# Performance work log

Hardware: AMD Instinct MI355X
Metric: run time of the kernel (lower is better)

The kernel has to match this reference:

```python
import jax, jax.numpy as jnp
import numpy as np

# ---- config (matches init_kwargs) ----
B, S, V = 8, 900, 11
H, NH, HD = 512, 8, 64          # hidden, heads, head_dim = H // NH
L = 2                            # num_layers
EXPANSION = 4.0
INNER = 1536                     # find_multiple(round(4.0 * 512 * 2/3), 256)
STEPS = 2                        # mcmc_num_steps
EPS = 1e-5                       # rms_norm_eps
THETA = 10000.0                  # rope_theta
ESCALE = float(np.sqrt(H))       # embed_scale = sqrt(hidden_size)
SCALE = 1.0 / float(np.sqrt(HD))


def rms_norm(x):
    return x * jax.lax.rsqrt(jnp.mean(x * x, axis=-1, keepdims=True) + EPS)


def rope_tables():
    inv_freq = 1.0 / (THETA ** (jnp.arange(0, HD, 2, dtype=jnp.float32) / HD))
    t = jnp.arange(S, dtype=jnp.float32)
    freqs = jnp.outer(t, inv_freq)                # (S, HD/2)
    emb = jnp.concatenate([freqs, freqs], axis=-1)  # (S, HD)
    return jnp.cos(emb), jnp.sin(emb)


def rotate_half(x):
    x1, x2 = jnp.split(x, 2, axis=-1)
    return jnp.concatenate([-x2, x1], axis=-1)


def apply_rope(q, k, cos, sin):
    cos = cos[None, :, None, :]  # (1,S,1,HD) broadcast over batch & heads
    sin = sin[None, :, None, :]
    return q * cos + rotate_half(q) * sin, k * cos + rotate_half(k) * sin


def block(h, qkv_w, o_w, gu_w, d_w, cos, sin):
    b, s, _ = h.shape
    qkv = (h @ qkv_w).reshape(b, s, 3 * NH, HD)
    q, k, v = qkv[:, :, :NH], qkv[:, :, NH:2 * NH], qkv[:, :, 2 * NH:]
    q, k = apply_rope(q, k, cos, sin)
    scores = jnp.einsum('bqhd,bkhd->bhqk', q, k) * SCALE
    attn = jax.nn.softmax(scores, axis=-1)
    out = jnp.einsum('bhqk,bkhd->bqhd', attn, v).reshape(b, s, NH * HD)
    h = rms_norm(h + out @ o_w)                   # post-norm residual
    gu = h @ gu_w
    gate, up = gu[..., :INNER], gu[..., INNER:]
    h = rms_norm(h + (jax.nn.silu(gate) * up) @ d_w)
    return h


def energy(logits, embed_w, energy_w, qkv_w, o_w, gu_w, d_w, input_emb, cos, sin):
    probs = jax.nn.softmax(logits, axis=-1)       # soft token distribution
    h = input_emb + ESCALE * (probs @ embed_w)    # soft embedding
    for i in range(L):
        h = block(h, qkv_w[i], o_w[i], gu_w[i], d_w[i], cos, sin)
    return jnp.sum(h @ energy_w)                  # scalar energy


def setup_inputs() -> dict:
    key = jax.random.key(0)
    ks = jax.random.split(key, 8)
    inputs = jax.random.randint(ks[0], (B, S), 0, V, dtype=jnp.int64)
    puzzle_identifiers = jax.random.randint(ks[1], (B,), 0, 1, dtype=jnp.int64)
    init_std = 1.0 / ESCALE
    embed_w = jax.random.normal(ks[2], (V, H), jnp.float32) * init_std
    energy_w = jax.random.normal(ks[3], (H, 1), jnp.float32) * 0.02
    qkv_w = jax.random.normal(ks[4], (L, H, 3 * NH * HD), jnp.float32) * 0.02
    o_w = jax.random.normal(ks[5], (L, NH * HD, H), jnp.float32) * 0.02
    gu_w = jax.random.normal(ks[6], (L, H, 2 * INNER), jnp.float32) * 0.02
    d_w = jax.random.normal(ks[7], (L, INNER, H), jnp.float32) * 0.02
    alpha = jnp.asarray(100.0, jnp.float32)       # mcmc_step_size
    return {"inputs": inputs, "puzzle_identifiers": puzzle_identifiers,
            "embed_w": embed_w, "energy_w": energy_w, "qkv_w": qkv_w,
            "o_w": o_w, "gu_w": gu_w, "d_w": d_w, "alpha": alpha}


def reference(inputs, puzzle_identifiers, embed_w, energy_w, qkv_w, o_w, gu_w, d_w, alpha):
    cos, sin = rope_tables()
    input_emb = ESCALE * embed_w[inputs]          # (B,S,H)
    a = jnp.maximum(alpha, 1e-4)                  # torch.clamp(alpha, min=1e-4)
    logits = jnp.zeros((inputs.shape[0], S, V), jnp.float32)
    egrad = jax.grad(energy)
    for _ in range(STEPS):                        # MCMC energy-descent loop
        g = egrad(logits, embed_w, energy_w, qkv_w, o_w, gu_w, d_w, input_emb, cos, sin)
        logits = logits - a * g
    return logits
```

## Files before the change

### kernel.cpp

```cpp
#include <hip/hip_runtime.h>
#include <math.h>

#define B_ 8
#define S_ 900
#define V_ 11
#define H_ 512
#define NH_ 8
#define HD_ 64
#define INNER_ 1536
#define STEPS_ 2
#define NTOK (B_*S_)
#define EPS_ 1e-5f
#define THETA_ 10000.0f
#define ESCALE_ 22.627416997969522f
#define SCALE_ 0.125f
#define PT_ 68

typedef __attribute__((ext_vector_type(8))) short bh8;
typedef __attribute__((ext_vector_type(4))) float f32x4;
typedef __attribute__((ext_vector_type(4))) unsigned short us4;

union bfu { bh8 v; unsigned short s[8]; us4 q[2]; };

__device__ inline unsigned short f2bf(float x) {
  unsigned u = __builtin_bit_cast(unsigned, x);
  return (unsigned short)((u + 0x7FFFu + ((u >> 16) & 1u)) >> 16);
}
__device__ inline float b2f(unsigned short s) {
  return __builtin_bit_cast(float, (unsigned)s << 16);
}

__device__ inline void gld16(const unsigned short* g, unsigned short* l) {
  __builtin_amdgcn_global_load_lds(
      (const __attribute__((address_space(1))) void*)(g),
      (__attribute__((address_space(3))) void*)(l), 16, 0, 0);
}

__device__ inline bh8 lds16(const unsigned short* p) {
  bfu u;
  u.q[0] = *(const us4*)p;
  u.q[1] = *(const us4*)(p + 4);
  return u.v;
}
__device__ inline void sts16(unsigned short* p, bfu u) {
  *(us4*)p = u.q[0];
  *(us4*)(p + 4) = u.q[1];
}

__device__ inline float wave_sum64(float x) {
#pragma unroll
  for (int off = 32; off > 0; off >>= 1) x += __shfl_xor(x, off, 64);
  return x;
}

__device__ inline float quad_sum(float x) {
  x += __shfl_xor(x, 1, 64);
  x += __shfl_xor(x, 2, 64);
  return x;
}


__global__ void k_zero(float* p, int n) {
  int i = blockIdx.x * blockDim.x + threadIdx.x;
  if (i < n) p[i] = 0.f;
}

__global__ void k_rope_tables(float* cs, float* sn) {
  int idx = blockIdx.x * blockDim.x + threadIdx.x;
  if (idx >= S_ * 32) return;
  int s = idx >> 5, i = idx & 31;
  float freq = powf(THETA_, -(float)i / 32.0f);
  float ang = (float)s * freq;
  cs[idx] = cosf(ang);
  sn[idx] = sinf(ang);
}

__global__ void k_softmax_logits(const float* __restrict__ logits, float* __restrict__ P) {
  int t = blockIdx.x * blockDim.x + threadIdx.x;
  if (t >= NTOK) return;
  float x[V_];
  float m = -1e30f;
#pragma unroll
  for (int v = 0; v < V_; ++v) { x[v] = logits[t * V_ + v]; m = fmaxf(m, x[v]); }
  float ssum = 0.f;
#pragma unroll
  for (int v = 0; v < V_; ++v) { x[v] = expf(x[v] - m); ssum += x[v]; }
  float inv = 1.f / ssum;
#pragma unroll
  for (int v = 0; v < V_; ++v) P[t * V_ + v] = x[v] * inv;
}

__global__ void k_h0(const float* __restrict__ P, const float* __restrict__ E,
                     const int* __restrict__ inp, float* __restrict__ h0,
                     unsigned short* __restrict__ h016) {
  int t = blockIdx.x;
  int tid = threadIdx.x;
  __shared__ float p[V_];
  __shared__ int iw;
  if (tid < V_) p[tid] = P[t * V_ + tid];
  if (tid == 0) iw = inp[t];
  __syncthreads();
  for (int h = tid; h < H_; h += blockDim.x) {
    float acc = E[iw * H_ + h];
#pragma unroll
    for (int v = 0; v < V_; ++v) acc += p[v] * E[v * H_ + h];
    float val = ESCALE_ * acc;
    h0[(size_t)t * H_ + h] = val;
    h016[(size_t)t * H_ + h] = f2bf(val);
  }
}

__global__ void k_gfill(const float* __restrict__ ew, float* __restrict__ G) {
  int idx = blockIdx.x * blockDim.x + threadIdx.x;
  if (idx < NTOK * H_) G[idx] = ew[idx & (H_ - 1)];
}

__global__ void k_cast8(const float* __restrict__ X, unsigned short* __restrict__ Y, int n8) {
  int i = blockIdx.x * blockDim.x + threadIdx.x;
  if (i >= n8) return;
  const float4* p = (const float4*)(X + (size_t)i * 8);
  float4 a = p[0], b = p[1];
  bfu o;
  o.s[0] = f2bf(a.x); o.s[1] = f2bf(a.y); o.s[2] = f2bf(a.z); o.s[3] = f2bf(a.w);
  o.s[4] = f2bf(b.x); o.s[5] = f2bf(b.y); o.s[6] = f2bf(b.z); o.s[7] = f2bf(b.w);
  *(bh8*)(Y + (size_t)i * 8) = o.v;
}


__global__ void k_wt(const float* __restrict__ W, unsigned short* __restrict__ WT, int K, int N) {
  __shared__ float t[32][33];
  int k0 = blockIdx.y * 32, n0 = blockIdx.x * 32;
  int tx = threadIdx.x, ty = threadIdx.y;
#pragma unroll
  for (int i = 0; i < 4; ++i)
    t[ty + 8 * i][tx] = W[(size_t)(k0 + ty + 8 * i) * N + n0 + tx];
  __syncthreads();
#pragma unroll
  for (int i = 0; i < 4; ++i)
    WT[(size_t)(n0 + ty + 8 * i) * K + k0 + tx] = f2bf(t[tx][ty + 8 * i]);
}


template <int SILU_A, int ADD, int CBF>
__global__ __launch_bounds__(256) void k_gemm(const unsigned short* __restrict__ A16,
                                              const unsigned short* __restrict__ Bt,
                                              const float* __restrict__ Dm,
                                              float* __restrict__ Cf,
                                              unsigned short* __restrict__ C16,
                                              int M, int N, int K, int lda) {
  __shared__ unsigned short As[64][32];
  __shared__ unsigned short Bs[128][32];
  int tid = threadIdx.x;
  int m0 = blockIdx.y * 64, n0 = blockIdx.x * 128;
  int wid = tid >> 6, lane = tid & 63;
  int wr = (wid >> 1) * 32, wc = (wid & 1) * 64;
  int lr = lane & 15, lg = lane >> 4;
  int srow = lane >> 2, sck = (lane & 3) * 8;
  f32x4 acc[2][4] = {};
  for (int k0 = 0; k0 < K; k0 += 32) {
    __syncthreads();
    if (SILU_A) {
      int row = tid >> 2, ck = (tid & 3) * 8;
      int gr = m0 + row; gr = gr < M ? gr : M - 1;
      const unsigned short* src = &A16[(size_t)gr * lda + k0 + ck];
      bfu pa;
#pragma unroll
      for (int j = 0; j < 8; ++j) {
        float g = b2f(src[j]), u = b2f(src[INNER_ + j]);
        pa.s[j] = f2bf((g / (1.f + __expf(-g))) * u);
      }
      *(bh8*)&As[row][ck] = pa.v;
    } else {
      int row = wid * 16 + srow;
      int gr = m0 + row; gr = gr < M ? gr : M - 1;
      gld16(&A16[(size_t)gr * lda + k0 + sck], &As[wid * 16][0]);
    }
#pragma unroll
    for (int i = 0; i < 2; ++i) {
      int bb = wid * 2 + i;
      gld16(&Bt[(size_t)(n0 + bb * 16 + srow) * K + k0 + sck], &Bs[bb * 16][0]);
    }
    __syncthreads();
    bh8 av[2], bv[4];
#pragma unroll
    for (int fr = 0; fr < 2; ++fr) av[fr] = *(const bh8*)&As[wr + fr * 16 + lr][lg * 8];
#pragma unroll
    for (int fc = 0; fc < 4; ++fc) bv[fc] = *(const bh8*)&Bs[wc + fc * 16 + lr][lg * 8];
#pragma unroll
    for (int fr = 0; fr < 2; ++fr)
#pragma unroll
      for (int fc = 0; fc < 4; ++fc)
        acc[fr][fc] = __builtin_amdgcn_mfma_f32_16x16x32_bf16(av[fr], bv[fc], acc[fr][fc], 0, 0, 0);
  }
#pragma unroll
  for (int fr = 0; fr < 2; ++fr) {
    int r0 = m0 + wr + fr * 16 + lg * 4;
#pragma unroll
    for (int i = 0; i < 4; ++i) {
      int gr = r0 + i;
      if (gr >= M) continue;
#pragma unroll
      for (int fc = 0; fc < 4; ++fc) {
        int gc = n0 + wc + fc * 16 + lr;
        float out = acc[fr][fc][i];
        if (ADD) out += Dm[(size_t)gr * N + gc];
        if (CBF) C16[(size_t)gr * N + gc] = f2bf(out);
        else Cf[(size_t)gr * N + gc] = out;
      }
    }
  }
}


template <int BWD>
__global__ void k_rope(unsigned short* __restrict__ Q, const float* __restrict__ cs,
                       const float* __restrict__ sn) {
  int idx = blockIdx.x * blockDim.x + threadIdx.x;
  if (idx >= NTOK * NH_ * 2 * 32) return;
  int i = idx & 31;
  int h = (idx >> 5) & (NH_ - 1);
  int part = (idx >> 8) & 1;
  int t = idx >> 9;
  int s = t % S_;
  float c = cs[s * 32 + i], sv = sn[s * 32 + i];
  size_t base = ((size_t)t * 3 * NH_ + part * NH_ + h) * HD_;
  float x1 = b2f(Q[base + i]), x2 = b2f(Q[base + 32 + i]);
  if (!BWD) {
    Q[base + i] = f2bf(x1 * c - x2 * sv);
    Q[base + 32 + i] = f2bf(x2 * c + x1 * sv);
  } else {
    Q[base + i] = f2bf(x1 * c + x2 * sv);
    Q[base + 32 + i] = f2bf(x2 * c - x1 * sv);
  }
}


__global__ __launch_bounds__(256) void k_attn_fwd3(const unsigned short* __restrict__ QKV,
                                                   unsigned short* __restrict__ AO,
                                                   float* __restrict__ MB,
                                                   float* __restrict__ LB) {
  __shared__ unsigned short Ks[64][PT_];
  __shared__ unsigned short VT[64][PT_];
  __shared__ unsigned short Ps[4][16][PT_];
  int tid = threadIdx.x;
  int h = blockIdx.y, b = blockIdx.z;
  int w = tid >> 6, lane = tid & 63;
  int lr = lane & 15, lg = lane >> 4;
  int q0 = blockIdx.x * 64 + w * 16;

  bh8 qf[2];
  {
    int qr = q0 + lr; if (qr >= S_) qr = S_ - 1;
    const unsigned short* qp = &QKV[((size_t)(b * S_ + qr) * 24 + h) * 64 + lg * 8];
    qf[0] = *(const bh8*)qp;
    qf[1] = *(const bh8*)(qp + 32);
  }
  f32x4 accO[4] = {};
  float m[4], lsum[4];
#pragma unroll
  for (int i = 0; i < 4; ++i) { m[i] = -1e30f; lsum[i] = 0.f; }

  for (int kt = 0; kt < S_; kt += 64) {
    __syncthreads();
    {
      int r = tid >> 2, c0 = (tid & 3) * 16;
      int src = kt + r;
      size_t ts = (size_t)b * S_ + (src < S_ ? src : S_ - 1);
      const unsigned short* gp = &QKV[(ts * 24 + 8 + h) * 64 + c0];
      bfu p0, p1;
      p0.v = *(const bh8*)gp;
      p1.v = *(const bh8*)(gp + 8);
      sts16(&Ks[r][c0], p0);
      sts16(&Ks[r][c0 + 8], p1);
    }
    {
      int d0 = (tid & 15) * 4, k0r = (tid >> 4) * 4;
      us4 rv[4];
#pragma unroll
      for (int j = 0; j < 4; ++j) {
        int src = kt + k0r + j;
        size_t ts = (size_t)b * S_ + (src < S_ ? src : S_ - 1);
        rv[j] = *(const us4*)&QKV[(ts * 24 + 16 + h) * 64 + d0];
      }
#pragma unroll
      for (int dd = 0; dd < 4; ++dd) {
        us4 pk = {rv[0][dd], rv[1][dd], rv[2][dd], rv[3][dd]};
        *(us4*)&VT[d0 + dd][k0r] = pk;
      }
    }
    __syncthreads();
    f32x4 accS[4] = {};
#pragma unroll
    for (int ks = 0; ks < 2; ++ks)
#pragma unroll
      for (int fk = 0; fk < 4; ++fk)
        accS[fk] = __builtin_amdgcn_mfma_f32_16x16x32_bf16(qf[ks], lds16(&Ks[fk * 16 + lr][ks * 32 + lg * 8]), accS[fk], 0, 0, 0);
    float sc[4][4], pmax[4];
#pragma unroll
    for (int i = 0; i < 4; ++i) pmax[i] = -1e30f;
#pragma unroll
    for (int fk = 0; fk < 4; ++fk)
#pragma unroll
      for (int i = 0; i < 4; ++i) {
        float s = accS[fk][i] * SCALE_;
        if (kt + fk * 16 + lr >= S_) s = -1e30f;
        sc[fk][i] = s;
        pmax[i] = fmaxf(pmax[i], s);
      }
#pragma unroll
    for (int i = 0; i < 4; ++i) {
      float v = pmax[i];
      v = fmaxf(v, __shfl_xor(v, 1, 64));
      v = fmaxf(v, __shfl_xor(v, 2, 64));
      v = fmaxf(v, __shfl_xor(v, 4, 64));
      v = fmaxf(v, __shfl_xor(v, 8, 64));
      pmax[i] = v;
    }
    float psum[4];
#pragma unroll
    for (int i = 0; i < 4; ++i) {
      float mn = fmaxf(m[i], pmax[i]);
      float eo = __expf(m[i] - mn);
      m[i] = mn;
      lsum[i] *= eo;
#pragma unroll
      for (int fd = 0; fd < 4; ++fd) accO[fd][i] *= eo;
      psum[i] = 0.f;
    }
#pragma unroll
    for (int fk = 0; fk < 4; ++fk)
#pragma unroll
      for (int i = 0; i < 4; ++i) {
        float p = __expf(sc[fk][i] - m[i]);
        sc[fk][i] = p;
        psum[i] += p;
      }
#pragma unroll
    for (int i = 0; i < 4; ++i) {
      float v = psum[i];
      v += __shfl_xor(v, 1, 64);
      v += __shfl_xor(v, 2, 64);
      v += __shfl_xor(v, 4, 64);
      v += __shfl_xor(v, 8, 64);
      lsum[i] += v;
    }
#pragma unroll
    for (int fk = 0; fk < 4; ++fk)
#pragma unroll
      for (int i = 0; i < 4; ++i)
        Ps[w][lg * 4 + i][fk * 16 + lr] = f2bf(sc[fk][i]);
#pragma unroll
    for (int ks = 0; ks < 2; ++ks) {
      bh8 ap = lds16(&Ps[w][lr][ks * 32 + lg * 8]);
#pragma unroll
      for (int fd = 0; fd < 4; ++fd)
        accO[fd] = __builtin_amdgcn_mfma_f32_16x16x32_bf16(ap, lds16(&VT[fd * 16 + lr][ks * 32 + lg * 8]), accO[fd], 0, 0, 0);
    }
  }
#pragma unroll
  for (int i = 0; i < 4; ++i) {
    int q = q0 + lg * 4 + i;
    if (q < S_) {
      float linv = 1.f / lsum[i];
      size_t obase = (size_t)(b * S_ + q) * H_ + h * 64;
#pragma unroll
      for (int fd = 0; fd < 4; ++fd) AO[obase + fd * 16 + lr] = f2bf(accO[fd][i] * linv);
      if (lr == 0) {
        MB[((size_t)b * NH_ + h) * S_ + q] = m[i];
        LB[((size_t)b * NH_ + h) * S_ + q] = linv;
      }
    }
  }
}

__global__ __launch_bounds__(256) void k_delta(const unsigned short* __restrict__ O,
                                               const unsigned short* __restrict__ dO,
                                               float* __restrict__ DB) {
  int tid = threadIdx.x;
  int h = blockIdx.y, b = blockIdx.z;
  int r = blockIdx.x * 64 + (tid >> 2), part = tid & 3;
  if (r >= S_) return;
  size_t base = (size_t)(b * S_ + r) * H_ + h * 64 + part * 16;
  bfu o0, o1, d0, d1;
  o0.v = *(const bh8*)&O[base];  o1.v = *(const bh8*)&O[base + 8];
  d0.v = *(const bh8*)&dO[base]; d1.v = *(const bh8*)&dO[base + 8];
  float s = 0.f;
#pragma unroll
  for (int j = 0; j < 8; ++j)
    s += b2f(o0.s[j]) * b2f(d0.s[j]) + b2f(o1.s[j]) * b2f(d1.s[j]);
  s = quad_sum(s);
  if (part == 0) DB[((size_t)b * NH_ + h) * S_ + r] = s;
}

__global__ __launch_bounds__(256) void k_attn_bwd_dq3(const unsigned short* __restrict__ QKV,
                                                      const unsigned short* __restrict__ dO,
                                                      const float* __restrict__ MB,
                                                      const float* __restrict__ LB,
                                                      const float* __restrict__ DB,
                                                      unsigned short* __restrict__ dQKV) {
  __shared__ unsigned short Ks[64][PT_];
  __shared__ unsigned short Vs[64][PT_];
  __shared__ unsigned short KT[64][PT_];
  __shared__ unsigned short Ps[4][16][PT_];
  int tid = threadIdx.x;
  int h = blockIdx.y, b = blockIdx.z;
  int w = tid >> 6, lane = tid & 63;
  int lr = lane & 15, lg = lane >> 4;
  int q0 = blockIdx.x * 64 + w * 16;
  size_t sbase = ((size_t)b * NH_ + h) * S_;

  bh8 qf[2], dof[2];
  {
    int qr = q0 + lr; if (qr >= S_) qr = S_ - 1;
    const unsigned short* qp = &QKV[((size_t)(b * S_ + qr) * 24 + h) * 64 + lg * 8];
    const unsigned short* dp = &dO[(size_t)(b * S_ + qr) * H_ + h * 64 + lg * 8];
    qf[0] = *(const bh8*)qp;  qf[1] = *(const bh8*)(qp + 32);
    dof[0] = *(const bh8*)dp; dof[1] = *(const bh8*)(dp + 32);
  }
  float mrow[4], lrow[4], drow[4];
#pragma unroll
  for (int i = 0; i < 4; ++i) {
    int q = q0 + lg * 4 + i; if (q >= S_) q = S_ - 1;
    mrow[i] = MB[sbase + q];
    lrow[i] = LB[sbase + q];
    drow[i] = DB[sbase + q];
  }
  f32x4 accQ[4] = {};

  for (int kt = 0; kt < S_; kt += 64) {
    __syncthreads();
    {
      int r = tid >> 2, c0 = (tid & 3) * 16;
      int src = kt + r;
      bool vld = src < S_;
      size_t ts = (size_t)b * S_ + (vld ? src : S_ - 1);
      const unsigned short* kp = &QKV[(ts * 24 + 8 + h) * 64 + c0];
      bfu p0{}, p1{}, p2{}, p3{};
      if (vld) {
        p0.v = *(const bh8*)kp;
        p1.v = *(const bh8*)(kp + 8);
        p2.v = *(const bh8*)(kp + 512);
        p3.v = *(const bh8*)(kp + 520);
      }
      sts16(&Ks[r][c0], p0); sts16(&Ks[r][c0 + 8], p1);
      sts16(&Vs[r][c0], p2); sts16(&Vs[r][c0 + 8], p3);
    }
    {
      int d0 = (tid & 15) * 4, k0r = (tid >> 4) * 4;
      us4 rv[4];
#pragma unroll
      for (int j = 0; j < 4; ++j) {
        int src = kt + k0r + j;
        bool vld = src < S_;
        size_t ts = (size_t)b * S_ + (vld ? src : S_ - 1);
        us4 t = *(const us4*)&QKV[(ts * 24 + 8 + h) * 64 + d0];
        if (!vld) t = us4{0, 0, 0, 0};
        rv[j] = t;
      }
#pragma unroll
      for (int dd = 0; dd < 4; ++dd) {
        us4 pk = {rv[0][dd], rv[1][dd], rv[2][dd], rv[3][dd]};
        *(us4*)&KT[d0 + dd][k0r] = pk;
      }
    }
    __syncthreads();
    f32x4 aS[4] = {}, aD[4] = {};
#pragma unroll
    for (int ks = 0; ks < 2; ++ks)
#pragma unroll
      for (int fk = 0; fk < 4; ++fk) {
        aS[fk] = __builtin_amdgcn_mfma_f32_16x16x32_bf16(qf[ks], lds16(&Ks[fk * 16 + lr][ks * 32 + lg * 8]), aS[fk], 0, 0, 0);
        aD[fk] = __builtin_amdgcn_mfma_f32_16x16x32_bf16(dof[ks], lds16(&Vs[fk * 16 + lr][ks * 32 + lg * 8]), aD[fk], 0, 0, 0);
      }
#pragma unroll
    for (int fk = 0; fk < 4; ++fk)
#pragma unroll
      for (int i = 0; i < 4; ++i) {
        float p = __expf(aS[fk][i] * SCALE_ - mrow[i]) * lrow[i];
        float ds = p * (aD[fk][i] - drow[i]);
        Ps[w][lg * 4 + i][fk * 16 + lr] = f2bf(ds);
      }
#pragma unroll
    for (int ks = 0; ks < 2; ++ks) {
      bh8 ap = lds16(&Ps[w][lr][ks * 32 + lg * 8]);
#pragma unroll
      for (int fd = 0; fd < 4; ++fd)
        accQ[fd] = __builtin_amdgcn_mfma_f32_16x16x32_bf16(ap, lds16(&KT[fd * 16 + lr][ks * 32 + lg * 8]), accQ[fd], 0, 0, 0);
    }
  }
#pragma unroll
  for (int i = 0; i < 4; ++i) {
    int q = q0 + lg * 4 + i;
    if (q < S_) {
      size_t obase = ((size_t)(b * S_ + q) * 24 + h) * 64;
#pragma unroll
      for (int fd = 0; fd < 4; ++fd) dQKV[obase + fd * 16 + lr] = f2bf(SCALE_ * accQ[fd][i]);
    }
  }
}

__global__ __launch_bounds__(256) void k_attn_bwd_kv3(const unsigned short* __restrict__ QKV,
                                                      const unsigned short* __restrict__ dO,
                                                      const float* __restrict__ MB,
                                                      const float* __restrict__ LB,
                                                      const float* __restrict__ DB,
                                                      unsigned short* __restrict__ dQKV) {
  __shared__ unsigned short Qs[64][PT_];
  __shared__ unsigned short dOs[64][PT_];
  __shared__ unsigned short QT[64][PT_];
  __shared__ unsigned short dOT[64][PT_];
  __shared__ unsigned short Ps[4][16][PT_];
  __shared__ float sM[64], sL[64], sD[64];
  int tid = threadIdx.x;
  int h = blockIdx.y, b = blockIdx.z;
  int w = tid >> 6, lane = tid & 63;
  int lr = lane & 15, lg = lane >> 4;
  int k0w = blockIdx.x * 64 + w * 16;
  size_t sbase = ((size_t)b * NH_ + h) * S_;

  bh8 kf[2], vf[2];
  {
    int kr = k0w + lr; if (kr >= S_) kr = S_ - 1;
    const unsigned short* kp = &QKV[((size_t)(b * S_ + kr) * 24 + 8 + h) * 64 + lg * 8];
    kf[0] = *(const bh8*)kp;        kf[1] = *(const bh8*)(kp + 32);
    vf[0] = *(const bh8*)(kp + 512); vf[1] = *(const bh8*)(kp + 544);
  }
  f32x4 accK[4] = {}, accV[4] = {};

  for (int qt = 0; qt < S_; qt += 64) {
    __syncthreads();
    {
      int r = tid >> 2, c0 = (tid & 3) * 16;
      int src = qt + r;
      bool vld = src < S_;
      size_t ts = (size_t)b * S_ + (vld ? src : S_ - 1);
      const unsigned short* qp = &QKV[(ts * 24 + h) * 64 + c0];
      const unsigned short* dp = &dO[ts * H_ + h * 64 + c0];
      bfu p0, p1, p2{}, p3{};
      p0.v = *(const bh8*)qp;
      p1.v = *(const bh8*)(qp + 8);
      if (vld) {
        p2.v = *(const bh8*)dp;
        p3.v = *(const bh8*)(dp + 8);
      }
      sts16(&Qs[r][c0], p0);  sts16(&Qs[r][c0 + 8], p1);
      sts16(&dOs[r][c0], p2); sts16(&dOs[r][c0 + 8], p3);
    }
    {
      int d0 = (tid & 15) * 4, q0r = (tid >> 4) * 4;
      us4 rq[4], rd[4];
#pragma unroll
      for (int j = 0; j < 4; ++j) {
        int src = qt + q0r + j;
        bool vld = src < S_;
        size_t ts = (size_t)b * S_ + (vld ? src : S_ - 1);
        rq[j] = *(const us4*)&QKV[(ts * 24 + h) * 64 + d0];
        us4 td = *(const us4*)&dO[ts * H_ + h * 64 + d0];
        if (!vld) td = us4{0, 0, 0, 0};
        rd[j] = td;
      }
#pragma unroll
      for (int dd = 0; dd < 4; ++dd) {
        us4 pq = {rq[0][dd], rq[1][dd], rq[2][dd], rq[3][dd]};
        us4 pd = {rd[0][dd], rd[1][dd], rd[2][dd], rd[3][dd]};
        *(us4*)&QT[d0 + dd][q0r] = pq;
        *(us4*)&dOT[d0 + dd][q0r] = pd;
      }
    }
    if (tid < 64) {
      int src = qt + tid;
      bool vld = src < S_;
      int sc = vld ? src : S_ - 1;
      sM[tid] = MB[sbase + sc];
      sL[tid] = LB[sbase + sc];
      sD[tid] = vld ? DB[sbase + sc] : 0.f;
    }
    __syncthreads();
    f32x4 aS[4] = {}, aD[4] = {};
#pragma unroll
    for (int ks = 0; ks < 2; ++ks)
#pragma unroll
      for (int fq = 0; fq < 4; ++fq) {
        aS[fq] = __builtin_amdgcn_mfma_f32_16x16x32_bf16(kf[ks], lds16(&Qs[fq * 16 + lr][ks * 32 + lg * 8]), aS[fq], 0, 0, 0);
        aD[fq] = __builtin_amdgcn_mfma_f32_16x16x32_bf16(vf[ks], lds16(&dOs[fq * 16 + lr][ks * 32 + lg * 8]), aD[fq], 0, 0, 0);
      }
    float pv[4][4];
#pragma unroll
    for (int fq = 0; fq < 4; ++fq) {
      float mq = sM[fq * 16 + lr], lq = sL[fq * 16 + lr];
#pragma unroll
      for (int i = 0; i < 4; ++i) {
        float p = __expf(aS[fq][i] * SCALE_ - mq) * lq;
        pv[fq][i] = p;
        Ps[w][lg * 4 + i][fq * 16 + lr] = f2bf(p);
      }
    }
#pragma unroll
    for (int qs = 0; qs < 2; ++qs) {
      bh8 ap = lds16(&Ps[w][lr][qs * 32 + lg * 8]);
#pragma unroll
      for (int fd = 0; fd < 4; ++fd)
        accV[fd] = __builtin_amdgcn_mfma_f32_16x16x32_bf16(ap, lds16(&dOT[fd * 16 + lr][qs * 32 + lg * 8]), accV[fd], 0, 0, 0);
    }
#pragma unroll
    for (int fq = 0; fq < 4; ++fq) {
      float dq = sD[fq * 16 + lr];
#pragma unroll
      for (int i = 0; i < 4; ++i)
        Ps[w][lg * 4 + i][fq * 16 + lr] = f2bf(pv[fq][i] * (aD[fq][i] - dq));
    }
#pragma unroll
    for (int qs = 0; qs < 2; ++qs) {
      bh8 ap = lds16(&Ps[w][lr][qs * 32 + lg * 8]);
#pragma unroll
      for (int fd = 0; fd < 4; ++fd)
        accK[fd] = __builtin_amdgcn_mfma_f32_16x16x32_bf16(ap, lds16(&QT[fd * 16 + lr][qs * 32 + lg * 8]), accK[fd], 0, 0, 0);
    }
  }
#pragma unroll
  for (int i = 0; i < 4; ++i) {
    int k = k0w + lg * 4 + i;
    if (k < S_) {
      size_t obase = ((size_t)(b * S_ + k) * 24 + 8 + h) * 64;
#pragma unroll
      for (int fd = 0; fd < 4; ++fd) {
        dQKV[obase + fd * 16 + lr] = f2bf(SCALE_ * accK[fd][i]);
        dQKV[obase + 512 + fd * 16 + lr] = f2bf(accV[fd][i]);
      }
    }
  }
}


__global__ __launch_bounds__(256) void k_rms_fwd(const float* __restrict__ X, float* __restrict__ Y,
                                                 unsigned short* __restrict__ Y16) {
  int t = blockIdx.x, tid = threadIdx.x;
  float x0 = X[(size_t)t * H_ + tid], x1 = X[(size_t)t * H_ + tid + 256];
  __shared__ float red[256];
  red[tid] = x0 * x0 + x1 * x1;
  __syncthreads();
  for (int s = 128; s > 0; s >>= 1) {
    if (tid < s) red[tid] += red[tid + s];
    __syncthreads();
  }
  float r = rsqrtf(red[0] / H_ + EPS_);
  float y0 = x0 * r, y1 = x1 * r;
  Y[(size_t)t * H_ + tid] = y0;
  Y[(size_t)t * H_ + tid + 256] = y1;
  Y16[(size_t)t * H_ + tid] = f2bf(y0);
  Y16[(size_t)t * H_ + tid + 256] = f2bf(y1);
}

__global__ __launch_bounds__(256) void k_rms_bwd(const float* __restrict__ X,
                                                 const float* __restrict__ GY,
                                                 float* __restrict__ GX,
                                                 unsigned short* __restrict__ GX16) {
  int t = blockIdx.x, tid = threadIdx.x;
  float x0 = X[(size_t)t * H_ + tid], x1 = X[(size_t)t * H_ + tid + 256];
  float g0 = GY[(size_t)t * H_ + tid], g1 = GY[(size_t)t * H_ + tid + 256];
  __shared__ float r1[256], r2[256];
  r1[tid] = x0 * x0 + x1 * x1;
  r2[tid] = x0 * g0 + x1 * g1;
  __syncthreads();
  for (int s = 128; s > 0; s >>= 1) {
    if (tid < s) { r1[tid] += r1[tid + s]; r2[tid] += r2[tid + s]; }
    __syncthreads();
  }
  float r = rsqrtf(r1[0] / H_ + EPS_);
  float coef = r * r * r * r2[0] / (float)H_;
  float o0 = r * g0 - coef * x0, o1 = r * g1 - coef * x1;
  GX[(size_t)t * H_ + tid] = o0;
  GX[(size_t)t * H_ + tid + 256] = o1;
  GX16[(size_t)t * H_ + tid] = f2bf(o0);
  GX16[(size_t)t * H_ + tid + 256] = f2bf(o1);
}


__global__ void k_silu_bwd(unsigned short* __restrict__ GU, const float* __restrict__ dact) {
  int idx = blockIdx.x * blockDim.x + threadIdx.x;
  if (idx >= NTOK * INNER_ / 8) return;
  int t = idx / (INNER_ / 8), i8 = (idx % (INNER_ / 8)) * 8;
  size_t gb = (size_t)t * 2 * INNER_;
  bfu g8, u8, og, ou;
  g8.v = *(const bh8*)&GU[gb + i8];
  u8.v = *(const bh8*)&GU[gb + INNER_ + i8];
  const float* da = &dact[(size_t)t * INNER_ + i8];
#pragma unroll
  for (int j = 0; j < 8; ++j) {
    float g = b2f(g8.s[j]), u = b2f(u8.s[j]), d = da[j];
    float sig = 1.f / (1.f + __expf(-g));
    og.s[j] = f2bf(d * u * sig * (1.f + g * (1.f - sig)));
    ou.s[j] = f2bf(d * g * sig);
  }
  *(bh8*)&GU[gb + i8] = og.v;
  *(bh8*)&GU[gb + INNER_ + i8] = ou.v;
}


__global__ __launch_bounds__(64) void k_logits_update(const float* __restrict__ G,
                                                      const float* __restrict__ E,
                                                      const float* __restrict__ P,
                                                      const float* __restrict__ alpha,
                                                      float* __restrict__ logits) {
  int t = blockIdx.x, lane = threadIdx.x;
  float dp[V_];
#pragma unroll
  for (int v = 0; v < V_; ++v) dp[v] = 0.f;
  for (int hh = lane; hh < H_; hh += 64) {
    float gh = G[(size_t)t * H_ + hh];
#pragma unroll
    for (int v = 0; v < V_; ++v) dp[v] += gh * E[v * H_ + hh];
  }
#pragma unroll
  for (int v = 0; v < V_; ++v) dp[v] = wave_sum64(dp[v]) * ESCALE_;
  float dot = 0.f;
  float pv[V_];
#pragma unroll
  for (int v = 0; v < V_; ++v) {
    pv[v] = P[t * V_ + v];
    dot += pv[v] * dp[v];
  }
  float a = fmaxf(alpha[0], 1e-4f);
  if (lane < V_) logits[t * V_ + lane] -= a * pv[lane] * (dp[lane] - dot);
}


struct Ctx {
  unsigned short *Q16, *Q016, *dQ16, *GU16, *DO16, *AO16, *AO016, *X116, *UDX16;
  float *ACT, *X1, *X2, *G, *UDX, *P, *MB, *LB, *DB, *MB0, *LB0, *CS, *SN;
  const unsigned short *WTqkv[2], *WTo[2], *WTgu[2], *WTd[2];
  const unsigned short *WSqkv[2], *WSo[2], *WSgu[2], *WSd[2];
  hipStream_t st;
};

static inline dim3 ggrid(int M, int N) { return dim3(N / 128, (M + 63) / 64); }

static void block_forward(Ctx& c, int l, const float* hin, const unsigned short* hin16,
                          float* hout, unsigned short* qb, unsigned short* ao,
                          float* mb, float* lb, bool skip_attn) {
  if (!skip_attn) {
    k_gemm<0, 0, 1><<<ggrid(NTOK, 3 * H_), 256, 0, c.st>>>(
        hin16, c.WTqkv[l], nullptr, nullptr, qb, NTOK, 3 * H_, H_, H_);
    k_rope<0><<<(NTOK * NH_ * 2 * 32 + 255) / 256, 256, 0, c.st>>>(qb, c.CS, c.SN);
    k_attn_fwd3<<<dim3((S_ + 63) / 64, NH_, B_), 256, 0, c.st>>>(qb, ao, mb, lb);
  }
  k_gemm<0, 1, 0><<<ggrid(NTOK, H_), 256, 0, c.st>>>(
      ao, c.WTo[l], hin, c.X1, nullptr, NTOK, H_, H_, H_);
  k_rms_fwd<<<NTOK, 256, 0, c.st>>>(c.X1, c.UDX, c.UDX16);
  k_gemm<0, 0, 1><<<ggrid(NTOK, 2 * INNER_), 256, 0, c.st>>>(
      c.UDX16, c.WTgu[l], nullptr, nullptr, c.GU16, NTOK, 2 * INNER_, H_, H_);
  k_gemm<1, 1, 0><<<ggrid(NTOK, H_), 256, 0, c.st>>>(
      c.GU16, c.WTd[l], c.UDX, c.X2, nullptr, NTOK, H_, INNER_, 2 * INNER_);
  if (hout) k_rms_fwd<<<NTOK, 256, 0, c.st>>>(c.X2, hout, c.UDX16);
}

static void block_backward(Ctx& c, int l, const float* hin, const unsigned short* hin16,
                           unsigned short* qb, unsigned short* ao, float* mb, float* lb,
                           bool skip_attn) {
  block_forward(c, l, hin, hin16, nullptr, qb, ao, mb, lb, skip_attn);
  k_rms_bwd<<<NTOK, 256, 0, c.st>>>(c.X2, c.G, c.UDX, c.UDX16);
  k_gemm<0, 0, 0><<<ggrid(NTOK, INNER_), 256, 0, c.st>>>(
      c.UDX16, c.WSd[l], nullptr, c.ACT, nullptr, NTOK, INNER_, H_, H_);
  k_silu_bwd<<<(NTOK * INNER_ / 8 + 255) / 256, 256, 0, c.st>>>(c.GU16, c.ACT);
  k_gemm<0, 1, 0><<<ggrid(NTOK, H_), 256, 0, c.st>>>(
      c.GU16, c.WSgu[l], c.UDX, c.G, nullptr, NTOK, H_, 2 * INNER_, 2 * INNER_);
  k_rms_bwd<<<NTOK, 256, 0, c.st>>>(c.X1, c.G, c.UDX, c.UDX16);
  k_gemm<0, 0, 1><<<ggrid(NTOK, H_), 256, 0, c.st>>>(
      c.UDX16, c.WSo[l], nullptr, nullptr, c.DO16, NTOK, H_, H_, H_);
  dim3 agrid((S_ + 63) / 64, NH_, B_);
  k_delta<<<agrid, 256, 0, c.st>>>(ao, c.DO16, c.DB);
  k_attn_bwd_dq3<<<agrid, 256, 0, c.st>>>(qb, c.DO16, mb, lb, c.DB, c.dQ16);
  k_attn_bwd_kv3<<<agrid, 256, 0, c.st>>>(qb, c.DO16, mb, lb, c.DB, c.dQ16);
  k_rope<1><<<(NTOK * NH_ * 2 * 32 + 255) / 256, 256, 0, c.st>>>(c.dQ16, c.CS, c.SN);
  k_gemm<0, 1, 0><<<ggrid(NTOK, H_), 256, 0, c.st>>>(
      c.dQ16, c.WSqkv[l], c.UDX, c.G, nullptr, NTOK, H_, 3 * H_, 3 * H_);
}

extern "C" void kernel_launch(void* const* d_in, const int* in_sizes, int n_in,
                              void* d_out, int out_size, void* d_ws, size_t ws_size,
                              hipStream_t stream) {
  const int* inputs = (const int*)d_in[0];
  const float* E = (const float*)d_in[2];
  const float* ew = (const float*)d_in[3];
  const float* qkvw = (const float*)d_in[4];
  const float* ow = (const float*)d_in[5];
  const float* guw = (const float*)d_in[6];
  const float* dw = (const float*)d_in[7];
  const float* alpha = (const float*)d_in[8];
  float* logits = (float*)d_out;

  const size_t WT_FLOATS = 3407872;
  const size_t NEED =
      2 * ((size_t)NTOK * 3 * H_ / 2) +
      ((size_t)NTOK * INNER_) +
      ((size_t)NTOK * INNER_) +
      4 * ((size_t)NTOK * H_) +
      2 * ((size_t)NTOK * H_ / 2) +
      3 * ((size_t)NTOK * H_ / 2) +
      ((size_t)NTOK * V_) +
      5 * ((size_t)B_ * NH_ * S_) +
      2 * ((size_t)S_ * 32) +
      2 * WT_FLOATS;
  if (ws_size < NEED * sizeof(float)) {
    k_zero<<<(NTOK * V_ + 255) / 256, 256, 0, stream>>>(logits, NTOK * V_);
    return;
  }

  float* f = (float*)d_ws;
  Ctx c;
  c.st = stream;
  c.Q16 = (unsigned short*)f;  f += (size_t)NTOK * 3 * H_ / 2;
  c.Q016 = (unsigned short*)f; f += (size_t)NTOK * 3 * H_ / 2;
  c.GU16 = (unsigned short*)f; f += (size_t)NTOK * INNER_;
  c.ACT = f; c.dQ16 = (unsigned short*)f; f += (size_t)NTOK * INNER_;
  c.X1 = f;   f += (size_t)NTOK * H_;
  c.X2 = f;   f += (size_t)NTOK * H_;
  c.G = f;    f += (size_t)NTOK * H_;
  c.UDX = f;  f += (size_t)NTOK * H_;
  c.AO16 = (unsigned short*)f;  f += (size_t)NTOK * H_ / 2;
  c.AO016 = (unsigned short*)f; f += (size_t)NTOK * H_ / 2;
  c.DO16 = (unsigned short*)f;  f += (size_t)NTOK * H_ / 2;
  c.X116 = (unsigned short*)f;  f += (size_t)NTOK * H_ / 2;
  c.UDX16 = (unsigned short*)f; f += (size_t)NTOK * H_ / 2;
  c.P = f;    f += (size_t)NTOK * V_;
  c.MB = f;   f += (size_t)B_ * NH_ * S_;
  c.LB = f;   f += (size_t)B_ * NH_ * S_;
  c.DB = f;   f += (size_t)B_ * NH_ * S_;
  c.MB0 = f;  f += (size_t)B_ * NH_ * S_;
  c.LB0 = f;  f += (size_t)B_ * NH_ * S_;
  c.CS = f;   f += (size_t)S_ * 32;
  c.SN = f;   f += (size_t)S_ * 32;
  unsigned short* wt = (unsigned short*)f;

  const size_t LQKV = (size_t)H_ * 3 * H_;
  const size_t LO = (size_t)H_ * H_;
  const size_t LGU = (size_t)H_ * 2 * INNER_;
  const size_t LD = (size_t)INNER_ * H_;

  for (int l = 0; l < 2; ++l) {
    c.WTqkv[l] = wt;
    k_wt<<<dim3(3 * H_ / 32, H_ / 32), dim3(32, 8), 0, stream>>>(qkvw + l * LQKV, wt, H_, 3 * H_);
    wt += LQKV;
    c.WTo[l] = wt;
    k_wt<<<dim3(H_ / 32, H_ / 32), dim3(32, 8), 0, stream>>>(ow + l * LO, wt, H_, H_);
    wt += LO;
    c.WTgu[l] = wt;
    k_wt<<<dim3(2 * INNER_ / 32, H_ / 32), dim3(32, 8), 0, stream>>>(guw + l * LGU, wt, H_, 2 * INNER_);
    wt += LGU;
    c.WTd[l] = wt;
    k_wt<<<dim3(H_ / 32, INNER_ / 32), dim3(32, 8), 0, stream>>>(dw + l * LD, wt, INNER_, H_);
    wt += LD;
  }
  {
    unsigned short* ws = wt;
    k_cast8<<<(int)((2 * LQKV / 8 + 255) / 256), 256, 0, stream>>>(qkvw, ws, (int)(2 * LQKV / 8));
    c.WSqkv[0] = ws; c.WSqkv[1] = ws + LQKV; ws += 2 * LQKV;
    k_cast8<<<(int)((2 * LO / 8 + 255) / 256), 256, 0, stream>>>(ow, ws, (int)(2 * LO / 8));
    c.WSo[0] = ws; c.WSo[1] = ws + LO; ws += 2 * LO;
    k_cast8<<<(int)((2 * LGU / 8 + 255) / 256), 256, 0, stream>>>(guw, ws, (int)(2 * LGU / 8));
    c.WSgu[0] = ws; c.WSgu[1] = ws + LGU; ws += 2 * LGU;
    k_cast8<<<(int)((2 * LD / 8 + 255) / 256), 256, 0, stream>>>(dw, ws, (int)(2 * LD / 8));
    c.WSd[0] = ws; c.WSd[1] = ws + LD;
  }

  k_zero<<<(NTOK * V_ + 255) / 256, 256, 0, stream>>>(logits, NTOK * V_);
  k_rope_tables<<<(S_ * 32 + 255) / 256, 256, 0, stream>>>(c.CS, c.SN);

  for (int step = 0; step < STEPS_; ++step) {
    k_softmax_logits<<<(NTOK + 255) / 256, 256, 0, stream>>>(logits, c.P);
    k_h0<<<NTOK, 256, 0, stream>>>(c.P, E, inputs, c.X1, c.X116);
    block_forward(c, 0, c.X1, c.X116, c.UDX, c.Q016, c.AO016, c.MB0, c.LB0, false);
    k_gfill<<<(NTOK * H_ + 255) / 256, 256, 0, stream>>>(ew, c.G);
    block_backward(c, 1, c.UDX, c.UDX16, c.Q16, c.AO16, c.MB, c.LB, false);
    k_h0<<<NTOK, 256, 0, stream>>>(c.P, E, inputs, c.X1, c.X116);
    block_backward(c, 0, c.X1, c.X116, c.Q016, c.AO016, c.MB0, c.LB0, true);
    k_logits_update<<<NTOK, 64, 0, stream>>>(c.G, E, c.P, alpha, logits);
  }
}
```

Measured before the change: 2.701 ms.

## Fuse RoPE and SiLU backward into GEMM and attention-backward epilogues

```diff
diff --git a/kernel.cpp b/kernel.cpp
--- a/kernel.cpp
+++ b/kernel.cpp
@@ -141,12 +141,15 @@
 }
 
 
-template <int SILU_A, int ADD, int CBF>
+template <int SILU_A, int ADD, int CBF, int ROPE, int SILUBWD>
 __global__ __launch_bounds__(256) void k_gemm(const unsigned short* __restrict__ A16,
                                               const unsigned short* __restrict__ Bt,
                                               const float* __restrict__ Dm,
                                               float* __restrict__ Cf,
                                               unsigned short* __restrict__ C16,
+                                              unsigned short* __restrict__ GU,
+                                              const float* __restrict__ Cs,
+                                              const float* __restrict__ Sn,
                                               int M, int N, int K, int lda) {
   __shared__ unsigned short As[64][32];
   __shared__ unsigned short Bs[128][32];
@@ -192,6 +195,7 @@
       for (int fc = 0; fc < 4; ++fc)
         acc[fr][fc] = __builtin_amdgcn_mfma_f32_16x16x32_bf16(av[fr], bv[fc], acc[fr][fc], 0, 0, 0);
   }
+  bool rope_on = ROPE && (((n0 + wc) >> 6) < 16);
 #pragma unroll
   for (int fr = 0; fr < 2; ++fr) {
     int r0 = m0 + wr + fr * 16 + lg * 4;
@@ -199,38 +203,38 @@
     for (int i = 0; i < 4; ++i) {
       int gr = r0 + i;
       if (gr >= M) continue;
+      float c0 = 1.f, s0 = 0.f, c1 = 1.f, s1 = 0.f;
+      if (ROPE) {
+        if (rope_on) {
+          int s = gr % S_;
+          c0 = Cs[s * 32 + lr];      s0 = Sn[s * 32 + lr];
+          c1 = Cs[s * 32 + 16 + lr]; s1 = Sn[s * 32 + 16 + lr];
+        }
+      }
 #pragma unroll
       for (int fc = 0; fc < 4; ++fc) {
         int gc = n0 + wc + fc * 16 + lr;
         float out = acc[fr][fc][i];
+        if (ROPE) {
+          float part = acc[fr][fc ^ 2][i];
+          float cc = (fc & 1) ? c1 : c0;
+          float ss = (fc & 1) ? s1 : s0;
+          out = (fc < 2) ? (out * cc - part * ss) : (out * cc + part * ss);
+        }
         if (ADD) out += Dm[(size_t)gr * N + gc];
-        if (CBF) C16[(size_t)gr * N + gc] = f2bf(out);
-        else Cf[(size_t)gr * N + gc] = out;
-      }
-    }
-  }
-}
-
-
-template <int BWD>
-__global__ void k_rope(unsigned short* __restrict__ Q, const float* __restrict__ cs,
-                       const float* __restrict__ sn) {
-  int idx = blockIdx.x * blockDim.x + threadIdx.x;
-  if (idx >= NTOK * NH_ * 2 * 32) return;
-  int i = idx & 31;
-  int h = (idx >> 5) & (NH_ - 1);
-  int part = (idx >> 8) & 1;
-  int t = idx >> 9;
-  int s = t % S_;
-  float c = cs[s * 32 + i], sv = sn[s * 32 + i];
-  size_t base = ((size_t)t * 3 * NH_ + part * NH_ + h) * HD_;
-  float x1 = b2f(Q[base + i]), x2 = b2f(Q[base + 32 + i]);
-  if (!BWD) {
-    Q[base + i] = f2bf(x1 * c - x2 * sv);
-    Q[base + 32 + i] = f2bf(x2 * c + x1 * sv);
-  } else {
-    Q[base + i] = f2bf(x1 * c + x2 * sv);
-    Q[base + 32 + i] = f2bf(x2 * c - x1 * sv);
+        if (SILUBWD) {
+          size_t gb = (size_t)gr * (size_t)(2 * INNER_) + gc;
+          float g = b2f(GU[gb]), u = b2f(GU[gb + INNER_]);
+          float sig = 1.f / (1.f + __expf(-g));
+          GU[gb] = f2bf(out * u * sig * (1.f + g * (1.f - sig)));
+          GU[gb + INNER_] = f2bf(out * g * sig);
+        } else if (CBF) {
+          C16[(size_t)gr * N + gc] = f2bf(out);
+        } else {
+          Cf[(size_t)gr * N + gc] = out;
+        }
+      }
+    }
   }
 }
 
@@ -397,6 +401,8 @@
                                                       const float* __restrict__ MB,
                                                       const float* __restrict__ LB,
                                                       const float* __restrict__ DB,
+                                                      const float* __restrict__ Cs,
+                                                      const float* __restrict__ Sn,
                                                       unsigned short* __restrict__ dQKV) {
   __shared__ unsigned short Ks[64][PT_];
   __shared__ unsigned short Vs[64][PT_];
@@ -493,8 +499,17 @@
     int q = q0 + lg * 4 + i;
     if (q < S_) {
       size_t obase = ((size_t)(b * S_ + q) * 24 + h) * 64;
-#pragma unroll
-      for (int fd = 0; fd < 4; ++fd) dQKV[obase + fd * 16 + lr] = f2bf(SCALE_ * accQ[fd][i]);
+      float c0 = Cs[q * 32 + lr], s0 = Sn[q * 32 + lr];
+      float c1 = Cs[q * 32 + 16 + lr], s1 = Sn[q * 32 + 16 + lr];
+#pragma unroll
+      for (int fd = 0; fd < 4; ++fd) {
+        float x = SCALE_ * accQ[fd][i];
+        float p = SCALE_ * accQ[fd ^ 2][i];
+        float cc = (fd & 1) ? c1 : c0;
+        float ss = (fd & 1) ? s1 : s0;
+        float out = (fd < 2) ? (x * cc + p * ss) : (x * cc - p * ss);
+        dQKV[obase + fd * 16 + lr] = f2bf(out);
+      }
     }
   }
 }
@@ -504,6 +519,8 @@
                                                       const float* __restrict__ MB,
                                                       const float* __restrict__ LB,
                                                       const float* __restrict__ DB,
+                                                      const float* __restrict__ Cs,
+                                                      const float* __restrict__ Sn,
                                                       unsigned short* __restrict__ dQKV) {
   __shared__ unsigned short Qs[64][PT_];
   __shared__ unsigned short dOs[64][PT_];
@@ -622,9 +639,16 @@
     int k = k0w + lg * 4 + i;
     if (k < S_) {
       size_t obase = ((size_t)(b * S_ + k) * 24 + 8 + h) * 64;
+      float c0 = Cs[k * 32 + lr], s0 = Sn[k * 32 + lr];
+      float c1 = Cs[k * 32 + 16 + lr], s1 = Sn[k * 32 + 16 + lr];
 #pragma unroll
       for (int fd = 0; fd < 4; ++fd) {
-        dQKV[obase + fd * 16 + lr] = f2bf(SCALE_ * accK[fd][i]);
+        float x = SCALE_ * accK[fd][i];
+        float p = SCALE_ * accK[fd ^ 2][i];
+        float cc = (fd & 1) ? c1 : c0;
+        float ss = (fd & 1) ? s1 : s0;
+        float out = (fd < 2) ? (x * cc + p * ss) : (x * cc - p * ss);
+        dQKV[obase + fd * 16 + lr] = f2bf(out);
         dQKV[obase + 512 + fd * 16 + lr] = f2bf(accV[fd][i]);
       }
     }
@@ -676,27 +700,6 @@
 }
 
 
-__global__ void k_silu_bwd(unsigned short* __restrict__ GU, const float* __restrict__ dact) {
-  int idx = blockIdx.x * blockDim.x + threadIdx.x;
-  if (idx >= NTOK * INNER_ / 8) return;
-  int t = idx / (INNER_ / 8), i8 = (idx % (INNER_ / 8)) * 8;
-  size_t gb = (size_t)t * 2 * INNER_;
-  bfu g8, u8, og, ou;
-  g8.v = *(const bh8*)&GU[gb + i8];
-  u8.v = *(const bh8*)&GU[gb + INNER_ + i8];
-  const float* da = &dact[(size_t)t * INNER_ + i8];
-#pragma unroll
-  for (int j = 0; j < 8; ++j) {
-    float g = b2f(g8.s[j]), u = b2f(u8.s[j]), d = da[j];
-    float sig = 1.f / (1.f + __expf(-g));
-    og.s[j] = f2bf(d * u * sig * (1.f + g * (1.f - sig)));
-    ou.s[j] = f2bf(d * g * sig);
-  }
-  *(bh8*)&GU[gb + i8] = og.v;
-  *(bh8*)&GU[gb + INNER_ + i8] = ou.v;
-}
-
-
 __global__ __launch_bounds__(64) void k_logits_update(const float* __restrict__ G,
                                                       const float* __restrict__ E,
                                                       const float* __restrict__ P,
@@ -727,7 +730,7 @@
 
 struct Ctx {
   unsigned short *Q16, *Q016, *dQ16, *GU16, *DO16, *AO16, *AO016, *X116, *UDX16;
-  float *ACT, *X1, *X2, *G, *UDX, *P, *MB, *LB, *DB, *MB0, *LB0, *CS, *SN;
+  float *X1, *X2, *G, *UDX, *P, *MB, *LB, *DB, *MB0, *LB0, *CS, *SN;
   const unsigned short *WTqkv[2], *WTo[2], *WTgu[2], *WTd[2];
   const unsigned short *WSqkv[2], *WSo[2], *WSgu[2], *WSd[2];
   hipStream_t st;
@@ -739,18 +742,17 @@
                           float* hout, unsigned short* qb, unsigned short* ao,
                           float* mb, float* lb, bool skip_attn) {
   if (!skip_attn) {
-    k_gemm<0, 0, 1><<<ggrid(NTOK, 3 * H_), 256, 0, c.st>>>(
-        hin16, c.WTqkv[l], nullptr, nullptr, qb, NTOK, 3 * H_, H_, H_);
-    k_rope<0><<<(NTOK * NH_ * 2 * 32 + 255) / 256, 256, 0, c.st>>>(qb, c.CS, c.SN);
+    k_gemm<0, 0, 1, 1, 0><<<ggrid(NTOK, 3 * H_), 256, 0, c.st>>>(
+        hin16, c.WTqkv[l], nullptr, nullptr, qb, nullptr, c.CS, c.SN, NTOK, 3 * H_, H_, H_);
     k_attn_fwd3<<<dim3((S_ + 63) / 64, NH_, B_), 256, 0, c.st>>>(qb, ao, mb, lb);
   }
-  k_gemm<0, 1, 0><<<ggrid(NTOK, H_), 256, 0, c.st>>>(
-      ao, c.WTo[l], hin, c.X1, nullptr, NTOK, H_, H_, H_);
+  k_gemm<0, 1, 0, 0, 0><<<ggrid(NTOK, H_), 256, 0, c.st>>>(
+      ao, c.WTo[l], hin, c.X1, nullptr, nullptr, nullptr, nullptr, NTOK, H_, H_, H_);
   k_rms_fwd<<<NTOK, 256, 0, c.st>>>(c.X1, c.UDX, c.UDX16);
-  k_gemm<0, 0, 1><<<ggrid(NTOK, 2 * INNER_), 256, 0, c.st>>>(
-      c.UDX16, c.WTgu[l], nullptr, nullptr, c.GU16, NTOK, 2 * INNER_, H_, H_);
-  k_gemm<1, 1, 0><<<ggrid(NTOK, H_), 256, 0, c.st>>>(
-      c.GU16, c.WTd[l], c.UDX, c.X2, nullptr, NTOK, H_, INNER_, 2 * INNER_);
+  k_gemm<0, 0, 1, 0, 0><<<ggrid(NTOK, 2 * INNER_), 256, 0, c.st>>>(
+      c.UDX16, c.WTgu[l], nullptr, nullptr, c.GU16, nullptr, nullptr, nullptr, NTOK, 2 * INNER_, H_, H_);
+  k_gemm<1, 1, 0, 0, 0><<<ggrid(NTOK, H_), 256, 0, c.st>>>(
+      c.GU16, c.WTd[l], c.UDX, c.X2, nullptr, nullptr, nullptr, nullptr, NTOK, H_, INNER_, 2 * INNER_);
   if (hout) k_rms_fwd<<<NTOK, 256, 0, c.st>>>(c.X2, hout, c.UDX16);
 }
 
@@ -759,21 +761,19 @@
                            bool skip_attn) {
   block_forward(c, l, hin, hin16, nullptr, qb, ao, mb, lb, skip_attn);
   k_rms_bwd<<<NTOK, 256, 0, c.st>>>(c.X2, c.G, c.UDX, c.UDX16);
-  k_gemm<0, 0, 0><<<ggrid(NTOK, INNER_), 256, 0, c.st>>>(
-      c.UDX16, c.WSd[l], nullptr, c.ACT, nullptr, NTOK, INNER_, H_, H_);
-  k_silu_bwd<<<(NTOK * INNER_ / 8 + 255) / 256, 256, 0, c.st>>>(c.GU16, c.ACT);
-  k_gemm<0, 1, 0><<<ggrid(NTOK, H_), 256, 0, c.st>>>(
-      c.GU16, c.WSgu[l], c.UDX, c.G, nullptr, NTOK, H_, 2 * INNER_, 2 * INNER_);
+  k_gemm<0, 0, 0, 0, 1><<<ggrid(NTOK, INNER_), 256, 0, c.st>>>(
+      c.UDX16, c.WSd[l], nullptr, nullptr, nullptr, c.GU16, nullptr, nullptr, NTOK, INNER_, H_, H_);
+  k_gemm<0, 1, 0, 0, 0><<<ggrid(NTOK, H_), 256, 0, c.st>>>(
+      c.GU16, c.WSgu[l], c.UDX, c.G, nullptr, nullptr, nullptr, nullptr, NTOK, H_, 2 * INNER_, 2 * INNER_);
   k_rms_bwd<<<NTOK, 256, 0, c.st>>>(c.X1, c.G, c.UDX, c.UDX16);
-  k_gemm<0, 0, 1><<<ggrid(NTOK, H_), 256, 0, c.st>>>(
-      c.UDX16, c.WSo[l], nullptr, nullptr, c.DO16, NTOK, H_, H_, H_);
+  k_gemm<0, 0, 1, 0, 0><<<ggrid(NTOK, H_), 256, 0, c.st>>>(
+      c.UDX16, c.WSo[l], nullptr, nullptr, c.DO16, nullptr, nullptr, nullptr, NTOK, H_, H_, H_);
   dim3 agrid((S_ + 63) / 64, NH_, B_);
   k_delta<<<agrid, 256, 0, c.st>>>(ao, c.DO16, c.DB);
-  k_attn_bwd_dq3<<<agrid, 256, 0, c.st>>>(qb, c.DO16, mb, lb, c.DB, c.dQ16);
-  k_attn_bwd_kv3<<<agrid, 256, 0, c.st>>>(qb, c.DO16, mb, lb, c.DB, c.dQ16);
-  k_rope<1><<<(NTOK * NH_ * 2 * 32 + 255) / 256, 256, 0, c.st>>>(c.dQ16, c.CS, c.SN);
-  k_gemm<0, 1, 0><<<ggrid(NTOK, H_), 256, 0, c.st>>>(
-      c.dQ16, c.WSqkv[l], c.UDX, c.G, nullptr, NTOK, H_, 3 * H_, 3 * H_);
+  k_attn_bwd_dq3<<<agrid, 256, 0, c.st>>>(qb, c.DO16, mb, lb, c.DB, c.CS, c.SN, c.dQ16);
+  k_attn_bwd_kv3<<<agrid, 256, 0, c.st>>>(qb, c.DO16, mb, lb, c.DB, c.CS, c.SN, c.dQ16);
+  k_gemm<0, 1, 0, 0, 0><<<ggrid(NTOK, H_), 256, 0, c.st>>>(
+      c.dQ16, c.WSqkv[l], c.UDX, c.G, nullptr, nullptr, nullptr, nullptr, NTOK, H_, 3 * H_, 3 * H_);
 }
 
 extern "C" void kernel_launch(void* const* d_in, const int* in_sizes, int n_in,
@@ -791,12 +791,10 @@
 
   const size_t WT_FLOATS = 3407872;
   const size_t NEED =
-      2 * ((size_t)NTOK * 3 * H_ / 2) +
-      ((size_t)NTOK * INNER_) +
+      3 * ((size_t)NTOK * 3 * H_ / 2) +
       ((size_t)NTOK * INNER_) +
       4 * ((size_t)NTOK * H_) +
-      2 * ((size_t)NTOK * H_ / 2) +
-      3 * ((size_t)NTOK * H_ / 2) +
+      5 * ((size_t)NTOK * H_ / 2) +
       ((size_t)NTOK * V_) +
       5 * ((size_t)B_ * NH_ * S_) +
       2 * ((size_t)S_ * 32) +
@@ -811,8 +809,8 @@
   c.st = stream;
   c.Q16 = (unsigned short*)f;  f += (size_t)NTOK * 3 * H_ / 2;
   c.Q016 = (unsigned short*)f; f += (size_t)NTOK * 3 * H_ / 2;
+  c.dQ16 = (unsigned short*)f; f += (size_t)NTOK * 3 * H_ / 2;
   c.GU16 = (unsigned short*)f; f += (size_t)NTOK * INNER_;
-  c.ACT = f; c.dQ16 = (unsigned short*)f; f += (size_t)NTOK * INNER_;
   c.X1 = f;   f += (size_t)NTOK * H_;
   c.X2 = f;   f += (size_t)NTOK * H_;
   c.G = f;    f += (size_t)NTOK * H_;
```

New measurement: 2.635 ms. 1.03x faster.
